# Optimization experiments

Hardware: AMD Instinct MI355X
Metric: run time of the kernel (lower is better)

## Reference

```python
import jax, jax.numpy as jnp
import numpy as np

N = 100000
E = 3200000
F_IN = 256
HID = 16
N_CLS = 32


def setup_inputs() -> dict:
    key = jax.random.key(0)
    ks = jax.random.split(key, 9)
    x = jax.random.normal(ks[0], (N, F_IN), dtype=jnp.float32)
    edge_index = jax.random.randint(ks[1], (2, E), 0, N, dtype=jnp.int32)
    def glorot(k, fan_in, fan_out):
        s = jnp.sqrt(6.0 / (fan_in + fan_out)).astype(jnp.float32)
        return jax.random.uniform(k, (fan_in, fan_out), jnp.float32, -s, s)
    return {
        "x": x,
        "edge_index": edge_index,
        "W1": glorot(ks[2], F_IN, HID), "b1": jnp.zeros((HID,), jnp.float32),
        "W2": glorot(ks[3], HID, HID), "b2": jnp.zeros((HID,), jnp.float32),
        "W3": glorot(ks[4], HID, N_CLS), "b3": jnp.zeros((N_CLS,), jnp.float32),
    }


def _gcn_conv(h, W, b, src, dst, deg_inv_sqrt):
    # h: [N, d_in] -> [N, d_out]. PyG GCNConv: linear, then D^-1/2 (A+I) D^-1/2 aggregation, then bias.
    h = h @ W                                        # [N, d_out]
    norm = deg_inv_sqrt[src] * deg_inv_sqrt[dst]     # [E]
    msg = h[src] * norm[:, None]                     # [E, d_out]
    agg = jax.ops.segment_sum(msg, dst, num_segments=N)
    # self-loop contribution: norm_ii = deg_inv_sqrt[i]^2
    agg = agg + (deg_inv_sqrt ** 2)[:, None] * h
    return agg + b


def reference(x, edge_index, W1, b1, W2, b2, W3, b3):
    src, dst = edge_index[0], edge_index[1]
    # degree with self-loops (edge weights = 1), computed on dst per PyG gcn_norm
    deg = jax.ops.segment_sum(jnp.ones((E,), jnp.float32), dst, num_segments=N) + 1.0
    deg_inv_sqrt = jax.lax.rsqrt(deg)
    h = jax.nn.elu(_gcn_conv(x, W1, b1, src, dst, deg_inv_sqrt))
    h = jax.nn.elu(_gcn_conv(h, W2, b2, src, dst, deg_inv_sqrt))
    h = jax.nn.elu(_gcn_conv(h, W3, b3, src, dst, deg_inv_sqrt))
    # dropout is identity in eval mode (training=False)
    return jax.nn.log_softmax(h, axis=1)
```

## Files before the change

kernel.cpp:

```cpp
#include <hip/hip_runtime.h>
#include <math.h>

static constexpr int N_NODES = 100000;
static constexpr int N_EDGES = 3200000;
static constexpr int F_INC   = 256;
static constexpr int HIDC    = 16;
static constexpr int NCLS    = 32;

static constexpr int BNODES  = 256;
static constexpr int NBKT    = (N_NODES + BNODES - 1) / BNODES;
static constexpr int CAP     = 9216;
static constexpr int CHUNK   = 4096;
static constexpr int NCHUNK  = (N_EDGES + CHUNK - 1) / CHUNK;

__device__ __forceinline__ unsigned pack_bf2(float a, float b) {
    unsigned ua = __float_as_uint(a);
    unsigned ub = __float_as_uint(b);
    ua = (ua + 0x7FFFu + ((ua >> 16) & 1u)) >> 16;
    ub = (ub + 0x7FFFu + ((ub >> 16) & 1u)) & 0xFFFF0000u;
    return ua | ub;
}
__device__ __forceinline__ float bflo(unsigned v) { return __uint_as_float(v << 16); }
__device__ __forceinline__ float bfhi(unsigned v) { return __uint_as_float(v & 0xFFFF0000u); }
__device__ __forceinline__ float elu1(float t) { return t > 0.f ? t : expm1f(t); }

__global__ void k_zero_cur(int* gcur) {
    int i = threadIdx.x;
    if (i < NBKT) gcur[i] = 0;
}

__global__ __launch_bounds__(256) void k_bucket(const int* __restrict__ src,
                                                const int* __restrict__ dst,
                                                int* gcur, unsigned int* __restrict__ slab) {
    __shared__ int hist[512];
    __shared__ int sc[512];
    __shared__ int place[512];
    __shared__ int gbase[512];
    __shared__ unsigned int staging[CHUNK];
    __shared__ unsigned short bid[CHUNK];
    int tid = threadIdx.x;
    int e0 = blockIdx.x * CHUNK;
    int n = min(CHUNK, N_EDGES - e0);
    hist[tid] = 0; hist[tid + 256] = 0;
    __syncthreads();
    unsigned int pay[16];
    int bk[16];
    #pragma unroll
    for (int r = 0; r < 16; ++r) {
        int i = r * 256 + tid;
        bk[r] = -1;
        if (i < n) {
            int e = e0 + i;
            int s = src[e];
            int t = dst[e];
            int b = t >> 8;
            pay[r] = (unsigned)s | ((unsigned)(t & 255) << 24);
            bk[r] = b;
            atomicAdd(&hist[b], 1);
        }
    }
    __syncthreads();
    sc[tid] = hist[tid]; sc[tid + 256] = hist[tid + 256];
    __syncthreads();
    for (int off = 1; off < 512; off <<= 1) {
        int i0 = tid, i1 = tid + 256;
        int v0 = (i0 >= off) ? sc[i0 - off] : 0;
        int v1 = (i1 >= off) ? sc[i1 - off] : 0;
        __syncthreads();
        sc[i0] += v0; sc[i1] += v1;
        __syncthreads();
    }
    {
        int b0 = tid, b1 = tid + 256;
        int o0 = sc[b0] - hist[b0];
        int o1 = sc[b1] - hist[b1];
        place[b0] = o0; place[b1] = o1;
        sc[b0] = o0; sc[b1] = o1;
        if (b0 < NBKT && hist[b0]) gbase[b0] = atomicAdd(&gcur[b0], hist[b0]);
        if (b1 < NBKT && hist[b1]) gbase[b1] = atomicAdd(&gcur[b1], hist[b1]);
    }
    __syncthreads();
    #pragma unroll
    for (int r = 0; r < 16; ++r) {
        if (bk[r] >= 0) {
            int p = atomicAdd(&place[bk[r]], 1);
            staging[p] = pay[r];
            bid[p] = (unsigned short)bk[r];
        }
    }
    __syncthreads();
    for (int i = tid; i < n; i += 256) {
        int b = bid[i];
        int gp = gbase[b] + (i - sc[b]);
        if (gp < CAP) slab[(size_t)b * CAP + gp] = staging[i];
    }
}

__global__ __launch_bounds__(512) void k_csr(const int* __restrict__ gcur,
                                             unsigned int* __restrict__ slab,
                                             int* __restrict__ rowptr,
                                             int* __restrict__ cnt,
                                             float* __restrict__ dis) {
    __shared__ int hist[BNODES];
    __shared__ int lofs[BNODES];
    __shared__ int place[BNODES];
    __shared__ unsigned int reord[CAP];
    int tid = threadIdx.x, b = blockIdx.x;
    if (tid < BNODES) hist[tid] = 0;
    __syncthreads();
    int count = min(gcur[b], CAP);
    unsigned int* sl = slab + (size_t)b * CAP;
    for (int i = tid; i < count; i += 512) atomicAdd(&hist[sl[i] >> 24], 1);
    __syncthreads();
    if (tid < BNODES) lofs[tid] = hist[tid];
    __syncthreads();
    for (int off = 1; off < BNODES; off <<= 1) {
        int v = 0;
        if (tid < BNODES && tid >= off) v = lofs[tid - off];
        __syncthreads();
        if (tid < BNODES) lofs[tid] += v;
        __syncthreads();
    }
    if (tid < BNODES) {
        int ex = lofs[tid] - hist[tid];
        lofs[tid] = ex;
        place[tid] = ex;
        int node = b * BNODES + tid;
        if (node < N_NODES) {
            rowptr[node] = b * CAP + ex;
            cnt[node] = hist[tid];
            dis[node] = rsqrtf((float)hist[tid] + 1.0f);
        }
    }
    __syncthreads();
    for (int i = tid; i < count; i += 512) {
        unsigned int v = sl[i];
        int dl = v >> 24;
        int p = atomicAdd(&place[dl], 1);
        reord[p] = v & 0xFFFFFFu;
    }
    __syncthreads();
    for (int i = tid; i < count; i += 512) sl[i] = reord[i];
}

__global__ __launch_bounds__(256) void k_linear1(const float* __restrict__ x,
                                                 const float* __restrict__ W1,
                                                 const float* __restrict__ dis,
                                                 unsigned* __restrict__ hb) {
    __shared__ float part[4][64][17];
    int tid = threadIdx.x;
    int lane = tid & 63;
    int w = __builtin_amdgcn_readfirstlane(tid >> 6);
    int node0 = blockIdx.x * 64;
    int n = node0 + lane;
    float acc[HIDC];
    #pragma unroll
    for (int j = 0; j < HIDC; ++j) acc[j] = 0.f;
    if (n < N_NODES) {
        const float4* xr = (const float4*)(x + (size_t)n * F_INC + w * 64);
        const float* wq = W1 + (size_t)w * 64 * HIDC;
        #pragma unroll
        for (int k4 = 0; k4 < 16; ++k4) {
            float4 v = xr[k4];
            const float* wk = wq + k4 * 4 * HIDC;
            #pragma unroll
            for (int j = 0; j < HIDC; ++j)
                acc[j] += v.x * wk[j] + v.y * wk[HIDC + j] + v.z * wk[2 * HIDC + j] + v.w * wk[3 * HIDC + j];
        }
    }
    #pragma unroll
    for (int j = 0; j < HIDC; ++j) part[w][lane][j] = acc[j];
    __syncthreads();
    int nl = tid >> 2;
    int jq = (tid & 3) * 4;
    int nn = node0 + nl;
    if (nn >= N_NODES) return;
    float s0 = part[0][nl][jq + 0] + part[1][nl][jq + 0] + part[2][nl][jq + 0] + part[3][nl][jq + 0];
    float s1 = part[0][nl][jq + 1] + part[1][nl][jq + 1] + part[2][nl][jq + 1] + part[3][nl][jq + 1];
    float s2 = part[0][nl][jq + 2] + part[1][nl][jq + 2] + part[2][nl][jq + 2] + part[3][nl][jq + 2];
    float s3 = part[0][nl][jq + 3] + part[1][nl][jq + 3] + part[2][nl][jq + 3] + part[3][nl][jq + 3];
    float dn = dis[nn];
    uint2 o = make_uint2(pack_bf2(dn * s0, dn * s1), pack_bf2(dn * s2, dn * s3));
    *(uint2*)(hb + (size_t)nn * 8 + (tid & 3) * 2) = o;
}

__device__ __forceinline__ void gather_core(int base, int deg, int q,
                                            const unsigned* __restrict__ csr,
                                            const unsigned* __restrict__ hb,
                                            unsigned sv, float& acc0, float& acc1) {
    acc0 = bflo(sv); acc1 = bfhi(sv);
    int j = 0;
    for (; j + 3 < deg; j += 4) {
        int s0 = csr[base + j];
        int s1 = csr[base + j + 1];
        int s2 = csr[base + j + 2];
        int s3 = csr[base + j + 3];
        unsigned v0 = hb[(size_t)s0 * 8 + q];
        unsigned v1 = hb[(size_t)s1 * 8 + q];
        unsigned v2 = hb[(size_t)s2 * 8 + q];
        unsigned v3 = hb[(size_t)s3 * 8 + q];
        acc0 += (bflo(v0) + bflo(v1)) + (bflo(v2) + bflo(v3));
        acc1 += (bfhi(v0) + bfhi(v1)) + (bfhi(v2) + bfhi(v3));
    }
    for (; j < deg; ++j) {
        int s = csr[base + j];
        unsigned v = hb[(size_t)s * 8 + q];
        acc0 += bflo(v);
        acc1 += bfhi(v);
    }
}

__global__ __launch_bounds__(256) void k_gather_fl1(const int* __restrict__ rowptr,
                                                    const int* __restrict__ cnt,
                                                    const unsigned* __restrict__ csr,
                                                    const float* __restrict__ dis,
                                                    const unsigned* __restrict__ hb,
                                                    const float* __restrict__ b1,
                                                    const float* __restrict__ W2,
                                                    unsigned* __restrict__ hb_out) {
    __shared__ float W2s[HIDC * HIDC];
    __shared__ float b1s[HIDC];
    if (threadIdx.x < HIDC * HIDC) W2s[threadIdx.x] = W2[threadIdx.x];
    if (threadIdx.x < HIDC) b1s[threadIdx.x] = b1[threadIdx.x];
    __syncthreads();
    int idx = blockIdx.x * blockDim.x + threadIdx.x;
    int n = idx >> 3;
    if (n >= N_NODES) return;
    int q = idx & 7;
    int lane = threadIdx.x & 63;
    float acc0, acc1;
    gather_core(rowptr[n], cnt[n], q, csr, hb, hb[(size_t)n * 8 + q], acc0, acc1);
    float dn = dis[n];
    float a0 = elu1(acc0 * dn + b1s[2 * q]);
    float a1 = elu1(acc1 * dn + b1s[2 * q + 1]);
    int gb = lane & 56;
    float h0 = 0.f, h1 = 0.f;
    #pragma unroll
    for (int k2 = 0; k2 < 8; ++k2) {
        float e0 = __shfl(a0, gb + k2, 64);
        float e1 = __shfl(a1, gb + k2, 64);
        h0 += e0 * W2s[(2 * k2) * HIDC + 2 * q]     + e1 * W2s[(2 * k2 + 1) * HIDC + 2 * q];
        h1 += e0 * W2s[(2 * k2) * HIDC + 2 * q + 1] + e1 * W2s[(2 * k2 + 1) * HIDC + 2 * q + 1];
    }
    hb_out[(size_t)n * 8 + q] = pack_bf2(dn * h0, dn * h1);
}

__global__ __launch_bounds__(256) void k_gather_z(const int* __restrict__ rowptr,
                                                  const int* __restrict__ cnt,
                                                  const unsigned* __restrict__ csr,
                                                  const float* __restrict__ dis,
                                                  const unsigned* __restrict__ hb,
                                                  const float* __restrict__ bias,
                                                  unsigned* __restrict__ outp) {
    int idx = blockIdx.x * blockDim.x + threadIdx.x;
    int n = idx >> 3;
    if (n >= N_NODES) return;
    int q = idx & 7;
    float acc0, acc1;
    gather_core(rowptr[n], cnt[n], q, csr, hb, hb[(size_t)n * 8 + q], acc0, acc1);
    float dn = dis[n];
    float z0 = elu1(acc0 * dn + bias[2 * q]);
    float z1 = elu1(acc1 * dn + bias[2 * q + 1]);
    outp[(size_t)n * 8 + q] = pack_bf2(dn * z0, dn * z1);
}

__global__ __launch_bounds__(256) void k_gather_fin(const int* __restrict__ rowptr,
                                                    const int* __restrict__ cnt,
                                                    const unsigned* __restrict__ csr,
                                                    const float* __restrict__ dis,
                                                    const unsigned* __restrict__ hb,
                                                    const float* __restrict__ W3,
                                                    const float* __restrict__ b3,
                                                    float* __restrict__ out) {
    __shared__ float W3s[HIDC * NCLS];
    __shared__ float b3s[NCLS];
    for (int i = threadIdx.x; i < HIDC * NCLS; i += 256) W3s[i] = W3[i];
    if (threadIdx.x < NCLS) b3s[threadIdx.x] = b3[threadIdx.x];
    __syncthreads();
    int idx = blockIdx.x * blockDim.x + threadIdx.x;
    int n = idx >> 3;
    if (n >= N_NODES) return;
    int q = idx & 7;
    int lane = threadIdx.x & 63;
    float acc0, acc1;
    gather_core(rowptr[n], cnt[n], q, csr, hb, hb[(size_t)n * 8 + q], acc0, acc1);
    float dn = dis[n];
    float g0 = acc0 * dn, g1 = acc1 * dn;
    int gb = lane & 56;
    int j0 = q * 4;
    float r0 = b3s[j0], r1 = b3s[j0 + 1], r2 = b3s[j0 + 2], r3 = b3s[j0 + 3];
    #pragma unroll
    for (int k2 = 0; k2 < 8; ++k2) {
        float e0 = __shfl(g0, gb + k2, 64);
        float e1 = __shfl(g1, gb + k2, 64);
        const float* wa = &W3s[(2 * k2) * NCLS + j0];
        const float* wb = &W3s[(2 * k2 + 1) * NCLS + j0];
        r0 += e0 * wa[0] + e1 * wb[0];
        r1 += e0 * wa[1] + e1 * wb[1];
        r2 += e0 * wa[2] + e1 * wb[2];
        r3 += e0 * wa[3] + e1 * wb[3];
    }
    r0 = elu1(r0); r1 = elu1(r1); r2 = elu1(r2); r3 = elu1(r3);
    float m = fmaxf(fmaxf(r0, r1), fmaxf(r2, r3));
    #pragma unroll
    for (int off = 1; off < 8; off <<= 1) m = fmaxf(m, __shfl_xor(m, off, 64));
    float s = expf(r0 - m) + expf(r1 - m) + expf(r2 - m) + expf(r3 - m);
    #pragma unroll
    for (int off = 1; off < 8; off <<= 1) s += __shfl_xor(s, off, 64);
    float lse = logf(s) + m;
    float4* o = (float4*)(out + (size_t)n * NCLS + j0);
    *o = make_float4(r0 - lse, r1 - lse, r2 - lse, r3 - lse);
}

extern "C" void kernel_launch(void* const* d_in, const int* in_sizes, int n_in,
                              void* d_out, int out_size, void* d_ws, size_t ws_size,
                              hipStream_t stream) {
    const float* x  = (const float*)d_in[0];
    const int*   ei = (const int*)d_in[1];
    const float* W1 = (const float*)d_in[2];
    const float* b1 = (const float*)d_in[3];
    const float* W2 = (const float*)d_in[4];
    const float* b2 = (const float*)d_in[5];
    const float* W3 = (const float*)d_in[6];
    const float* b3 = (const float*)d_in[7];
    float* out = (float*)d_out;
    const int* src = ei;
    const int* dst = ei + N_EDGES;

    int* wi = (int*)d_ws;
    int*          gcur   = wi;
    unsigned int* slab   = (unsigned int*)(wi + 512);
    int*          rowptr = wi + 512 + NBKT * CAP;
    int*          cnt    = rowptr + 102400;
    float*        dis    = (float*)(cnt + 102400);
    unsigned*     Bh     = (unsigned*)(dis + 102400);
    unsigned*     Zb     = Bh + 819200;
    (void)ws_size; (void)n_in; (void)in_sizes; (void)out_size;

    auto blocks = [](long long n) { return (int)((n + 255) / 256); };
    const int GGATH = blocks((long long)N_NODES * 8);
    const int GLIN1 = (N_NODES + 63) / 64;

    k_zero_cur<<<1, 512, 0, stream>>>(gcur);
    k_bucket<<<NCHUNK, 256, 0, stream>>>(src, dst, gcur, slab);
    k_csr<<<NBKT, 512, 0, stream>>>(gcur, slab, rowptr, cnt, dis);

    k_linear1<<<GLIN1, 256, 0, stream>>>(x, W1, dis, Bh);
    k_gather_fl1<<<GGATH, 256, 0, stream>>>(rowptr, cnt, slab, dis, Bh, b1, W2, Zb);
    k_gather_z<<<GGATH, 256, 0, stream>>>(rowptr, cnt, slab, dis, Zb, b2, Bh);
    k_gather_fin<<<GGATH, 256, 0, stream>>>(rowptr, cnt, slab, dis, Bh, W3, b3, out);
}
```

Measured before the change: 184.7 us.

## Compute first-layer linear with bf16 MFMA 16x16x32 per wavefront tile

Replaces the scalar FMA x@W1 kernel (4 waves splitting K, reduced through shared memory) with one 16-node tile per wavefront using bf16 MFMA instructions. Inputs and W1 are converted to bf16 in registers and accumulated in fp32. The result goes through per-wave LDS to produce packed bf16 outputs scaled by deg^-1/2. This cuts ALU work, but x is still read once, so the kernel stays bound by the 100MB input read. The change adds bf16 rounding of the inputs, and it syncs with a waitcnt instead of a barrier, relying on wave-local LDS.

```diff
diff --git a/kernel.cpp b/kernel.cpp
--- a/kernel.cpp
+++ b/kernel.cpp
@@ -12,6 +12,10 @@
 static constexpr int CAP     = 9216;
 static constexpr int CHUNK   = 4096;
 static constexpr int NCHUNK  = (N_EDGES + CHUNK - 1) / CHUNK;
+static constexpr int NTILES  = N_NODES / 16;
+
+typedef __attribute__((ext_vector_type(8))) short bf16x8;
+typedef __attribute__((ext_vector_type(4))) float f32x4;
 
 __device__ __forceinline__ unsigned pack_bf2(float a, float b) {
     unsigned ua = __float_as_uint(a);
@@ -147,41 +151,49 @@
                                                  const float* __restrict__ W1,
                                                  const float* __restrict__ dis,
                                                  unsigned* __restrict__ hb) {
-    __shared__ float part[4][64][17];
+    __shared__ float dtile[4][16][18];
     int tid = threadIdx.x;
     int lane = tid & 63;
-    int w = __builtin_amdgcn_readfirstlane(tid >> 6);
-    int node0 = blockIdx.x * 64;
-    int n = node0 + lane;
-    float acc[HIDC];
-    #pragma unroll
-    for (int j = 0; j < HIDC; ++j) acc[j] = 0.f;
-    if (n < N_NODES) {
-        const float4* xr = (const float4*)(x + (size_t)n * F_INC + w * 64);
-        const float* wq = W1 + (size_t)w * 64 * HIDC;
+    int w = tid >> 6;
+    int tile = blockIdx.x * 4 + w;
+    if (tile >= NTILES) return;
+    int g = lane >> 4;
+    int r = lane & 15;
+    union { uint4 u; bf16x8 v; } bfr[8];
+    #pragma unroll
+    for (int m = 0; m < 8; ++m) {
+        unsigned uu[4];
         #pragma unroll
-        for (int k4 = 0; k4 < 16; ++k4) {
-            float4 v = xr[k4];
-            const float* wk = wq + k4 * 4 * HIDC;
-            #pragma unroll
-            for (int j = 0; j < HIDC; ++j)
-                acc[j] += v.x * wk[j] + v.y * wk[HIDC + j] + v.z * wk[2 * HIDC + j] + v.w * wk[3 * HIDC + j];
+        for (int t = 0; t < 4; ++t) {
+            int k0 = 32 * m + 8 * g + 2 * t;
+            uu[t] = pack_bf2(W1[k0 * HIDC + r], W1[(k0 + 1) * HIDC + r]);
         }
-    }
-    #pragma unroll
-    for (int j = 0; j < HIDC; ++j) part[w][lane][j] = acc[j];
-    __syncthreads();
-    int nl = tid >> 2;
-    int jq = (tid & 3) * 4;
-    int nn = node0 + nl;
-    if (nn >= N_NODES) return;
-    float s0 = part[0][nl][jq + 0] + part[1][nl][jq + 0] + part[2][nl][jq + 0] + part[3][nl][jq + 0];
-    float s1 = part[0][nl][jq + 1] + part[1][nl][jq + 1] + part[2][nl][jq + 1] + part[3][nl][jq + 1];
-    float s2 = part[0][nl][jq + 2] + part[1][nl][jq + 2] + part[2][nl][jq + 2] + part[3][nl][jq + 2];
-    float s3 = part[0][nl][jq + 3] + part[1][nl][jq + 3] + part[2][nl][jq + 3] + part[3][nl][jq + 3];
-    float dn = dis[nn];
-    uint2 o = make_uint2(pack_bf2(dn * s0, dn * s1), pack_bf2(dn * s2, dn * s3));
-    *(uint2*)(hb + (size_t)nn * 8 + (tid & 3) * 2) = o;
+        bfr[m].u = make_uint4(uu[0], uu[1], uu[2], uu[3]);
+    }
+    const float* xrow = x + (size_t)(tile * 16 + r) * F_INC;
+    f32x4 acc = {0.f, 0.f, 0.f, 0.f};
+    #pragma unroll
+    for (int m = 0; m < 8; ++m) {
+        int ks = 32 * m + 8 * g;
+        float4 va = *(const float4*)(xrow + ks);
+        float4 vb = *(const float4*)(xrow + ks + 4);
+        union { uint4 u; bf16x8 v; } af;
+        af.u = make_uint4(pack_bf2(va.x, va.y), pack_bf2(va.z, va.w),
+                          pack_bf2(vb.x, vb.y), pack_bf2(vb.z, vb.w));
+        acc = __builtin_amdgcn_mfma_f32_16x16x32_bf16(af.v, bfr[m].v, acc, 0, 0, 0);
+    }
+    #pragma unroll
+    for (int t = 0; t < 4; ++t) dtile[w][4 * g + t][r] = acc[t];
+    __builtin_amdgcn_s_waitcnt(0);
+    int q = lane & 7;
+    #pragma unroll
+    for (int h = 0; h < 2; ++h) {
+        int rr = (lane >> 3) + 8 * h;
+        int node = tile * 16 + rr;
+        float dn = dis[node];
+        hb[(size_t)node * 8 + q] =
+            pack_bf2(dn * dtile[w][rr][2 * q], dn * dtile[w][rr][2 * q + 1]);
+    }
 }
 
 __device__ __forceinline__ void gather_core(int base, int deg, int q,
@@ -339,7 +351,7 @@
 
     auto blocks = [](long long n) { return (int)((n + 255) / 256); };
     const int GGATH = blocks((long long)N_NODES * 8);
-    const int GLIN1 = (N_NODES + 63) / 64;
+    const int GLIN1 = (NTILES + 3) / 4;
 
     k_zero_cur<<<1, 512, 0, stream>>>(gcur);
     k_bucket<<<NCHUNK, 256, 0, stream>>>(src, dst, gcur, slab);
```

Result: faster. 166.4 us (-9.9%).
